# Kernel tuning notes

Hardware: AMD Instinct MI355X
Metric: run time of the kernel (lower is better)

## Reference

```python
import jax, jax.numpy as jnp
import numpy as np
import math

B, T, C, H = 2, 2048, 1024, 16
HD = C // H

def setup_inputs() -> dict:
    key = jax.random.key(0)
    ks = jax.random.split(key, 5)
    s_in = 1.0 / math.sqrt(C)
    x = jax.random.normal(ks[0], (B, T, C), dtype=jnp.float32)
    W_attn = jax.random.normal(ks[1], (C, 3 * C), dtype=jnp.float32) * s_in
    b_attn = jnp.zeros((3 * C,), dtype=jnp.float32)
    W_proj = jax.random.normal(ks[2], (C, C), dtype=jnp.float32) * s_in
    b_proj = jnp.zeros((C,), dtype=jnp.float32)
    return {"x": x, "W_attn": W_attn, "b_attn": b_attn, "W_proj": W_proj, "b_proj": b_proj}

def reference(x, W_attn, b_attn, W_proj, b_proj):
    Bx, Tx, Cx = x.shape
    c = x @ W_attn + b_attn  # [B,T,3C]
    q, k, v = jnp.split(c, 3, axis=2)
    # [B,T,H,hd] -> [B,H,T,hd]
    q = q.reshape(Bx, Tx, H, HD).transpose(0, 2, 1, 3)
    k = k.reshape(Bx, Tx, H, HD).transpose(0, 2, 1, 3)
    v = v.reshape(Bx, Tx, H, HD).transpose(0, 2, 1, 3)
    # NOTE: module scales by 1/sqrt(C), not 1/sqrt(head_dim)
    attn = jnp.einsum('bhqd,bhkd->bhqk', q, k) * (1.0 / math.sqrt(Cx))
    causal = jnp.tril(jnp.ones((Tx, Tx), dtype=bool))
    attn = jnp.where(causal[None, None], attn, -jnp.inf)
    attn = jax.nn.softmax(attn, axis=-1)
    y = jnp.einsum('bhqk,bhkd->bhqd', attn, v)
    y = y.transpose(0, 2, 1, 3).reshape(Bx, Tx, Cx)
    return y @ W_proj + b_proj
```

## Files before the change

### kernel.cpp

```cpp
#include <hip/hip_runtime.h>
#include <math.h>

#define Bv 2
#define Tv 2048
#define Cv 1024
#define Hv 16
#define HDv 64
#define Mv (Bv * Tv)
#define SZv (Bv * Hv * Tv * HDv)

typedef short bf16x8 __attribute__((ext_vector_type(8)));
typedef float f32x4 __attribute__((ext_vector_type(4)));

static __device__ __forceinline__ unsigned short f2bf(float f) {
    unsigned u = __float_as_uint(f);
    u += 0x7fffu + ((u >> 16) & 1u);
    return (unsigned short)(u >> 16);
}

static __device__ __forceinline__ unsigned f2bf2(float a, float b) {
    unsigned r;
    asm("v_cvt_pk_bf16_f32 %0, %1, %2" : "=v"(r) : "v"(a), "v"(b));
    return r;
}

#define AS1 __attribute__((address_space(1)))
#define AS3 __attribute__((address_space(3)))
#define GLD16(gp, lp) __builtin_amdgcn_global_load_lds( \
    (AS1 const void*)(const void*)(gp), (AS3 void*)(void*)(lp), 16, 0, 0)

#define WAITVM(n) asm volatile("s_waitcnt vmcnt(" #n ")" ::: "memory")
#define WAITLGKM0 asm volatile("s_waitcnt lgkmcnt(0)" ::: "memory")
#define BARRIER   asm volatile("s_barrier" ::: "memory")

__global__ __launch_bounds__(256) void cvt_kernel(
    const float* __restrict__ src, unsigned short* __restrict__ dst, int n4)
{
    int i = blockIdx.x * 256 + threadIdx.x;
    if (i < n4) {
        float4 f = ((const float4*)src)[i];
        ushort4 u;
        u.x = f2bf(f.x); u.y = f2bf(f.y); u.z = f2bf(f.z); u.w = f2bf(f.w);
        ((ushort4*)dst)[i] = u;
    }
}

__global__ __launch_bounds__(256) void transpose_kernel(
    const float* __restrict__ src, unsigned short* __restrict__ dst,
    int R, int Ncols)
{
    __shared__ float tile[32][33];
    const int c0 = blockIdx.x * 32, r0 = blockIdx.y * 32;
    const int tx = threadIdx.x & 31, ty = threadIdx.x >> 5;
    #pragma unroll
    for (int i = 0; i < 4; ++i)
        tile[ty + i * 8][tx] = src[(size_t)(r0 + ty + i * 8) * Ncols + c0 + tx];
    __syncthreads();
    #pragma unroll
    for (int i = 0; i < 4; ++i)
        dst[(size_t)(c0 + ty + i * 8) * R + r0 + tx] = f2bf(tile[tx][ty + i * 8]);
}

__device__ __forceinline__ void mm_mainloop_1024(
    const unsigned short* __restrict__ A, const unsigned short* __restrict__ Bt,
    unsigned short* lds, int rowBase, int colBase, f32x4 acc[4][4])
{
    const int tid  = threadIdx.x;
    const int lane = tid & 63;
    const int w    = tid >> 6;
    const int quad = lane >> 4, l15 = lane & 15;
    const int wm = (w >> 1) * 64, wn = (w & 1) * 64;
    const int K = 1024;

    const int g0 = (w * 2 + 0) * 64 + lane;
    const int g1 = (w * 2 + 1) * 64 + lane;
    const int r0 = g0 >> 2, r1 = g1 >> 2;
    const int kc0 = (g0 & 3) ^ ((r0 >> 1) & 3);
    const int kc1 = (g1 & 3) ^ ((r1 >> 1) & 3);
    const size_t offA0 = (size_t)(rowBase + r0) * K + kc0 * 8;
    const size_t offA1 = (size_t)(rowBase + r1) * K + kc1 * 8;
    const size_t offB0 = (size_t)(colBase + r0) * K + kc0 * 8;
    const size_t offB1 = (size_t)(colBase + r1) * K + kc1 * 8;
    unsigned short* ldsA0 = lds + (w * 2 + 0) * 512;
    unsigned short* ldsA1 = lds + (w * 2 + 1) * 512;
    unsigned short* ldsB0 = lds + 4096 + (w * 2 + 0) * 512;
    unsigned short* ldsB1 = lds + 4096 + (w * 2 + 1) * 512;

    const int sw = quad ^ ((l15 >> 1) & 3);
    int aoff[4], boff[4];
    #pragma unroll
    for (int i = 0; i < 4; ++i) {
        aoff[i] = ((wm + i * 16 + l15) * 4 + sw) * 8;
        boff[i] = 4096 + ((wn + i * 16 + l15) * 4 + sw) * 8;
    }

    GLD16(A + offA0, ldsA0);
    GLD16(A + offA1, ldsA1);
    GLD16(Bt + offB0, ldsB0);
    GLD16(Bt + offB1, ldsB1);

    for (int i = 0; i < 32; ++i) {
        const int cur = (i & 1) * 8192;
        const int nxt = 8192 - cur;
        if (i < 31) {
            const int k1 = (i + 1) * 32;
            GLD16(A + offA0 + k1, ldsA0 + nxt);
            GLD16(A + offA1 + k1, ldsA1 + nxt);
            GLD16(Bt + offB0 + k1, ldsB0 + nxt);
            GLD16(Bt + offB1 + k1, ldsB1 + nxt);
            WAITVM(4);
        } else {
            WAITVM(0);
        }
        BARRIER;

        bf16x8 a[4], b[4];
        #pragma unroll
        for (int j = 0; j < 4; ++j) a[j] = *(const bf16x8*)(lds + cur + aoff[j]);
        #pragma unroll
        for (int j = 0; j < 4; ++j) b[j] = *(const bf16x8*)(lds + cur + boff[j]);

        #pragma unroll
        for (int mi = 0; mi < 4; ++mi)
            #pragma unroll
            for (int ni = 0; ni < 4; ++ni)
                acc[mi][ni] = __builtin_amdgcn_mfma_f32_16x16x32_bf16(
                    a[mi], b[ni], acc[mi][ni], 0, 0, 0);

        WAITLGKM0;
        BARRIER;
    }
}

__global__ __launch_bounds__(256) void qkv_mm_kernel(
    const unsigned short* __restrict__ xB, const unsigned short* __restrict__ WaT,
    const float* __restrict__ bias,
    unsigned short* __restrict__ qB, unsigned short* __restrict__ kB,
    unsigned short* __restrict__ vT)
{
    __shared__ __align__(16) unsigned short lds[128 * 136];
    const int rowBase = blockIdx.y * 128;
    const int colBase = blockIdx.x * 128;

    f32x4 acc[4][4];
    #pragma unroll
    for (int i = 0; i < 4; ++i)
        #pragma unroll
        for (int j = 0; j < 4; ++j) acc[i][j] = (f32x4){0.f, 0.f, 0.f, 0.f};

    mm_mainloop_1024(xB, WaT, lds, rowBase, colBase, acc);
    __syncthreads();

    const int tid = threadIdx.x, lane = tid & 63, w = tid >> 6;
    const int quad = lane >> 4, l15 = lane & 15;
    const int wm = (w >> 1) * 64, wn = (w & 1) * 64;
    const int s = colBase / Cv;
    const int tloc = rowBase & (Tv - 1);
    const int bh0 = (rowBase / Tv) * Hv + (colBase % Cv) / HDv;

    if (s < 2) {
        const float qs = (s == 0) ? 0.04508422f : 1.0f;
        #pragma unroll
        for (int mi = 0; mi < 4; ++mi)
            #pragma unroll
            for (int ni = 0; ni < 4; ++ni) {
                float bv = bias[colBase + wn + ni * 16 + l15];
                #pragma unroll
                for (int r = 0; r < 4; ++r) {
                    int m = wm + mi * 16 + quad * 4 + r;
                    int n = wn + ni * 16 + l15;
                    lds[m * 136 + n] = f2bf((acc[mi][ni][r] + bv) * qs);
                }
            }
        __syncthreads();
        unsigned short* dst = (s == 0) ? qB : kB;
        #pragma unroll
        for (int it = 0; it < 8; ++it) {
            int cc = tid + it * 256;
            int m = cc >> 4, j = cc & 15;
            uint4 v = *(const uint4*)(lds + m * 136 + j * 8);
            int hh = j >> 3, d0 = (j & 7) * 8;
            *(uint4*)(dst + ((size_t)(bh0 + hh) * Tv + tloc + m) * HDv + d0) = v;
        }
    } else {
        #pragma unroll
        for (int mi = 0; mi < 4; ++mi)
            #pragma unroll
            for (int ni = 0; ni < 4; ++ni) {
                float bv = bias[colBase + wn + ni * 16 + l15];
                #pragma unroll
                for (int r = 0; r < 4; ++r) {
                    int m = wm + mi * 16 + quad * 4 + r;
                    int n = wn + ni * 16 + l15;
                    lds[n * 136 + m] = f2bf(acc[mi][ni][r] + bv);
                }
            }
        __syncthreads();
        #pragma unroll
        for (int it = 0; it < 8; ++it) {
            int cc = tid + it * 256;
            int n = cc >> 4, j = cc & 15;
            uint4 v = *(const uint4*)(lds + n * 136 + j * 8);
            int hh = n >> 6, d = n & 63;
            *(uint4*)(vT + ((size_t)(bh0 + hh) * HDv + d) * Tv + tloc + j * 8) = v;
        }
    }
}

__global__ __launch_bounds__(256) void proj_mm_kernel(
    const unsigned short* __restrict__ y0B, const unsigned short* __restrict__ WpT,
    const float* __restrict__ bias, float* __restrict__ out)
{
    __shared__ __align__(16) unsigned short lds[16384];
    const int rowBase = blockIdx.y * 128;
    const int colBase = blockIdx.x * 128;

    f32x4 acc[4][4];
    #pragma unroll
    for (int i = 0; i < 4; ++i)
        #pragma unroll
        for (int j = 0; j < 4; ++j) acc[i][j] = (f32x4){0.f, 0.f, 0.f, 0.f};

    mm_mainloop_1024(y0B, WpT, lds, rowBase, colBase, acc);

    const int tid = threadIdx.x, lane = tid & 63, w = tid >> 6;
    const int quad = lane >> 4, l15 = lane & 15;
    const int wm = (w >> 1) * 64, wn = (w & 1) * 64;

    #pragma unroll
    for (int mi = 0; mi < 4; ++mi)
        #pragma unroll
        for (int ni = 0; ni < 4; ++ni) {
            int n = colBase + wn + ni * 16 + l15;
            float bv = bias[n];
            #pragma unroll
            for (int r = 0; r < 4; ++r) {
                int m = rowBase + wm + mi * 16 + quad * 4 + r;
                out[(size_t)m * Cv + n] = acc[mi][ni][r] + bv;
            }
        }
}

__global__ __launch_bounds__(256) void attn_kernel(
    const unsigned short* __restrict__ qB, const unsigned short* __restrict__ kB,
    const unsigned short* __restrict__ vT, unsigned short* __restrict__ y0B)
{
    __shared__ __align__(16) unsigned short kv[2 * 8192];
    __shared__ __align__(16) unsigned short Pb[4][16 * 72];

    const int tid  = threadIdx.x;
    const int lane = tid & 63;
    const int w    = tid >> 6;
    const int quad = lane >> 4;
    const int l15  = lane & 15;

    const int qt = 31 - (blockIdx.x >> 5);
    const int bh = blockIdx.x & 31;
    const int qwbase = qt * 64 + w * 16;

    const unsigned short* qrow = qB + ((size_t)bh * Tv + qwbase + l15) * HDv;
    const bf16x8 Qa0 = *(const bf16x8*)(qrow + quad * 8);
    const bf16x8 Qa1 = *(const bf16x8*)(qrow + 32 + quad * 8);
    WAITVM(0);

    f32x4 O[4];
    float l[4] = {0.f, 0.f, 0.f, 0.f};
    #pragma unroll
    for (int n = 0; n < 4; ++n) O[n] = (f32x4){0.f, 0.f, 0.f, 0.f};

    const unsigned short* Kbase = kB + (size_t)bh * Tv * HDv;
    const unsigned short* Vbase = vT + (size_t)bh * HDv * Tv;
    unsigned short* Pw = &Pb[w][0];

    const unsigned short* gK[2]; unsigned short* dK[2];
    const unsigned short* gV[2]; unsigned short* dV[2];
    #pragma unroll
    for (int i = 0; i < 2; ++i) {
        int slot = tid + i * 256;
        int row = slot >> 3;
        int gk = (slot & 7) ^ ((row >> 2) & 7);
        gK[i] = Kbase + row * HDv + gk * 8;
        dK[i] = kv + (size_t)(i * 256 + w * 64) * 8;
        int d = slot >> 3;
        int gv = (slot & 7) ^ (d & 7);
        gV[i] = Vbase + (size_t)d * Tv + gv * 8;
        dV[i] = kv + 4096 + (size_t)(i * 256 + w * 64) * 8;
    }

    int koff[4][2], voff[4][2];
    #pragma unroll
    for (int ct = 0; ct < 4; ++ct) {
        int row = ct + 4 * l15;
        #pragma unroll
        for (int j = 0; j < 2; ++j)
            koff[ct][j] = (row * 8 + ((quad + 4 * j) ^ (l15 & 7))) * 8;
    }
    #pragma unroll
    for (int nt = 0; nt < 4; ++nt) {
        int d = nt * 16 + l15;
        #pragma unroll
        for (int j = 0; j < 2; ++j)
            voff[nt][j] = 4096 + (d * 8 + ((quad + 4 * j) ^ (l15 & 7))) * 8;
    }

    GLD16(gK[0], dK[0]);
    GLD16(gK[1], dK[1]);
    GLD16(gV[0], dV[0]);
    GLD16(gV[1], dV[1]);

    for (int kt = 0; kt <= qt; ++kt) {
        const int cur = (kt & 1) * 8192;
        const int nxt = 8192 - cur;
        if (kt < qt) {
            const int kb1 = (kt + 1) * 64;
            GLD16(gK[0] + (size_t)kb1 * HDv, dK[0] + nxt);
            GLD16(gK[1] + (size_t)kb1 * HDv, dK[1] + nxt);
            GLD16(gV[0] + kb1, dV[0] + nxt);
            GLD16(gV[1] + kb1, dV[1] + nxt);
            WAITVM(4);
        } else {
            WAITVM(0);
        }
        BARRIER;

        bf16x8 Kb[4][2], Vb[4][2];
        #pragma unroll
        for (int ct = 0; ct < 4; ++ct) {
            Kb[ct][0] = *(const bf16x8*)(kv + cur + koff[ct][0]);
            Kb[ct][1] = *(const bf16x8*)(kv + cur + koff[ct][1]);
        }
        #pragma unroll
        for (int nt = 0; nt < 4; ++nt) {
            Vb[nt][0] = *(const bf16x8*)(kv + cur + voff[nt][0]);
            Vb[nt][1] = *(const bf16x8*)(kv + cur + voff[nt][1]);
        }

        f32x4 S[4];
        #pragma unroll
        for (int ct = 0; ct < 4; ++ct) {
            S[ct] = (f32x4){0.f, 0.f, 0.f, 0.f};
            S[ct] = __builtin_amdgcn_mfma_f32_16x16x32_bf16(Qa0, Kb[ct][0], S[ct], 0, 0, 0);
            S[ct] = __builtin_amdgcn_mfma_f32_16x16x32_bf16(Qa1, Kb[ct][1], S[ct], 0, 0, 0);
        }

        if (kt == qt) {
            #pragma unroll
            for (int ct = 0; ct < 4; ++ct)
                #pragma unroll
                for (int r = 0; r < 4; ++r)
                    if (ct + 4 * l15 > w * 16 + quad * 4 + r) S[ct][r] = -1e30f;
        }

        float p[4][4];
        #pragma unroll
        for (int ct = 0; ct < 4; ++ct)
            #pragma unroll
            for (int r = 0; r < 4; ++r)
                p[ct][r] = __builtin_amdgcn_exp2f(S[ct][r]);
        #pragma unroll
        for (int r = 0; r < 4; ++r)
            l[r] += (p[0][r] + p[1][r]) + (p[2][r] + p[3][r]);

        #pragma unroll
        for (int r = 0; r < 4; ++r) {
            uint2 u = make_uint2(f2bf2(p[0][r], p[1][r]), f2bf2(p[2][r], p[3][r]));
            *(uint2*)(Pw + (quad * 4 + r) * 72 + l15 * 4) = u;
        }
        WAITLGKM0;
        const bf16x8 Pa0 = *(const bf16x8*)(Pw + l15 * 72 + quad * 8);
        const bf16x8 Pa1 = *(const bf16x8*)(Pw + l15 * 72 + 32 + quad * 8);

        #pragma unroll
        for (int nt = 0; nt < 4; ++nt) {
            O[nt] = __builtin_amdgcn_mfma_f32_16x16x32_bf16(Pa0, Vb[nt][0], O[nt], 0, 0, 0);
            O[nt] = __builtin_amdgcn_mfma_f32_16x16x32_bf16(Pa1, Vb[nt][1], O[nt], 0, 0, 0);
        }

        WAITLGKM0;
        BARRIER;
    }

    #pragma unroll
    for (int r = 0; r < 4; ++r) {
        l[r] += __shfl_xor(l[r], 1);
        l[r] += __shfl_xor(l[r], 2);
        l[r] += __shfl_xor(l[r], 4);
        l[r] += __shfl_xor(l[r], 8);
    }

    const int b = bh >> 4, h = bh & 15;
    #pragma unroll
    for (int r = 0; r < 4; ++r) {
        float inv = 1.f / l[r];
        int q = qwbase + quad * 4 + r;
        unsigned short* dst = y0B + ((size_t)(b * Tv + q)) * Cv + h * HDv + l15;
        #pragma unroll
        for (int n = 0; n < 4; ++n) dst[n * 16] = f2bf(O[n][r] * inv);
    }
}

extern "C" void kernel_launch(void* const* d_in, const int* in_sizes, int n_in,
                              void* d_out, int out_size, void* d_ws, size_t ws_size,
                              hipStream_t stream) {
    const float* x      = (const float*)d_in[0];
    const float* W_attn = (const float*)d_in[1];
    const float* b_attn = (const float*)d_in[2];
    const float* W_proj = (const float*)d_in[3];
    const float* b_proj = (const float*)d_in[4];
    float* out = (float*)d_out;

    unsigned short* xB  = (unsigned short*)d_ws;
    unsigned short* WaT = xB  + (size_t)Mv * Cv;
    unsigned short* WpT = WaT + (size_t)3 * Cv * Cv;
    unsigned short* qB  = WpT + (size_t)Cv * Cv;
    unsigned short* kB  = qB + (size_t)SZv;
    unsigned short* vT  = kB + (size_t)SZv;
    unsigned short* y0B = vT + (size_t)SZv;

    dim3 blk(256);
    cvt_kernel<<<dim3((Mv * Cv / 4) / 256), blk, 0, stream>>>(x, xB, Mv * Cv / 4);
    transpose_kernel<<<dim3(3 * Cv / 32, Cv / 32), blk, 0, stream>>>(W_attn, WaT, Cv, 3 * Cv);
    transpose_kernel<<<dim3(Cv / 32, Cv / 32), blk, 0, stream>>>(W_proj, WpT, Cv, Cv);
    qkv_mm_kernel<<<dim3(3 * Cv / 128, Mv / 128), blk, 0, stream>>>(xB, WaT, b_attn, qB, kB, vT);
    attn_kernel<<<dim3(Bv * Hv * (Tv / 64)), blk, 0, stream>>>(qB, kB, vT, y0B);
    proj_mm_kernel<<<dim3(Cv / 128, Mv / 128), blk, 0, stream>>>(y0B, WpT, b_proj, out);
}
```

Before: 181.8 us.

## Triple-buffer GEMM LDS pipeline, single-barrier attention loop, merge prep kernels

```diff
diff --git a/kernel.cpp b/kernel.cpp
--- a/kernel.cpp
+++ b/kernel.cpp
@@ -33,32 +33,37 @@
 #define WAITLGKM0 asm volatile("s_waitcnt lgkmcnt(0)" ::: "memory")
 #define BARRIER   asm volatile("s_barrier" ::: "memory")
 
-__global__ __launch_bounds__(256) void cvt_kernel(
-    const float* __restrict__ src, unsigned short* __restrict__ dst, int n4)
+__global__ __launch_bounds__(256) void prep_kernel(
+    const float* __restrict__ x, const float* __restrict__ Wa,
+    const float* __restrict__ Wp,
+    unsigned short* __restrict__ xB, unsigned short* __restrict__ WaT,
+    unsigned short* __restrict__ WpT)
 {
-    int i = blockIdx.x * 256 + threadIdx.x;
-    if (i < n4) {
-        float4 f = ((const float4*)src)[i];
+    __shared__ float tile[32][33];
+    const int bid = blockIdx.x;
+    const int tid = threadIdx.x;
+
+    if (bid < 4096) {
+        int i = bid * 256 + tid;
+        float4 f = ((const float4*)x)[i];
         ushort4 u;
         u.x = f2bf(f.x); u.y = f2bf(f.y); u.z = f2bf(f.z); u.w = f2bf(f.w);
-        ((ushort4*)dst)[i] = u;
-    }
-}
-
-__global__ __launch_bounds__(256) void transpose_kernel(
-    const float* __restrict__ src, unsigned short* __restrict__ dst,
-    int R, int Ncols)
-{
-    __shared__ float tile[32][33];
-    const int c0 = blockIdx.x * 32, r0 = blockIdx.y * 32;
-    const int tx = threadIdx.x & 31, ty = threadIdx.x >> 5;
+        ((ushort4*)xB)[i] = u;
+        return;
+    }
+    const float* src; unsigned short* dst; int Ncols, bi;
+    if (bid < 7168) { bi = bid - 4096; Ncols = 3072; src = Wa; dst = WaT; }
+    else            { bi = bid - 7168; Ncols = 1024; src = Wp; dst = WpT; }
+    const int nct = Ncols / 32;
+    const int c0 = (bi % nct) * 32, r0 = (bi / nct) * 32;
+    const int tx = tid & 31, ty = tid >> 5;
     #pragma unroll
     for (int i = 0; i < 4; ++i)
         tile[ty + i * 8][tx] = src[(size_t)(r0 + ty + i * 8) * Ncols + c0 + tx];
     __syncthreads();
     #pragma unroll
     for (int i = 0; i < 4; ++i)
-        dst[(size_t)(c0 + ty + i * 8) * R + r0 + tx] = f2bf(tile[tx][ty + i * 8]);
+        dst[(size_t)(c0 + ty + i * 8) * Cv + r0 + tx] = f2bf(tile[tx][ty + i * 8]);
 }
 
 __device__ __forceinline__ void mm_mainloop_1024(
@@ -98,21 +103,23 @@
     GLD16(A + offA1, ldsA1);
     GLD16(Bt + offB0, ldsB0);
     GLD16(Bt + offB1, ldsB1);
-
+    GLD16(A + offA0 + 32, ldsA0 + 8192);
+    GLD16(A + offA1 + 32, ldsA1 + 8192);
+    GLD16(Bt + offB0 + 32, ldsB0 + 8192);
+    GLD16(Bt + offB1 + 32, ldsB1 + 8192);
+
+    int cur = 0;
     for (int i = 0; i < 32; ++i) {
-        const int cur = (i & 1) * 8192;
-        const int nxt = 8192 - cur;
-        if (i < 31) {
-            const int k1 = (i + 1) * 32;
-            GLD16(A + offA0 + k1, ldsA0 + nxt);
-            GLD16(A + offA1 + k1, ldsA1 + nxt);
-            GLD16(Bt + offB0 + k1, ldsB0 + nxt);
-            GLD16(Bt + offB1 + k1, ldsB1 + nxt);
-            WAITVM(4);
-        } else {
-            WAITVM(0);
-        }
+        if (i < 31) { WAITVM(4); } else { WAITVM(0); }
         BARRIER;
+        if (i < 30) {
+            int nb = cur + 16384; if (nb >= 24576) nb -= 24576;
+            const int k2 = (i + 2) * 32;
+            GLD16(A + offA0 + k2, ldsA0 + nb);
+            GLD16(A + offA1 + k2, ldsA1 + nb);
+            GLD16(Bt + offB0 + k2, ldsB0 + nb);
+            GLD16(Bt + offB1 + k2, ldsB1 + nb);
+        }
 
         bf16x8 a[4], b[4];
         #pragma unroll
@@ -127,8 +134,7 @@
                 acc[mi][ni] = __builtin_amdgcn_mfma_f32_16x16x32_bf16(
                     a[mi], b[ni], acc[mi][ni], 0, 0, 0);
 
-        WAITLGKM0;
-        BARRIER;
+        cur += 8192; if (cur == 24576) cur = 0;
     }
 }
 
@@ -138,7 +144,7 @@
     unsigned short* __restrict__ qB, unsigned short* __restrict__ kB,
     unsigned short* __restrict__ vT)
 {
-    __shared__ __align__(16) unsigned short lds[128 * 136];
+    __shared__ __align__(16) unsigned short lds[24576];
     const int rowBase = blockIdx.y * 128;
     const int colBase = blockIdx.x * 128;
 
@@ -211,7 +217,7 @@
     const unsigned short* __restrict__ y0B, const unsigned short* __restrict__ WpT,
     const float* __restrict__ bias, float* __restrict__ out)
 {
-    __shared__ __align__(16) unsigned short lds[16384];
+    __shared__ __align__(16) unsigned short lds[24576];
     const int rowBase = blockIdx.y * 128;
     const int colBase = blockIdx.x * 128;
 
@@ -308,20 +314,18 @@
     GLD16(gV[0], dV[0]);
     GLD16(gV[1], dV[1]);
 
+    int cur = 0;
     for (int kt = 0; kt <= qt; ++kt) {
-        const int cur = (kt & 1) * 8192;
-        const int nxt = 8192 - cur;
+        WAITVM(0);
+        BARRIER;
         if (kt < qt) {
             const int kb1 = (kt + 1) * 64;
+            const int nxt = 8192 - cur;
             GLD16(gK[0] + (size_t)kb1 * HDv, dK[0] + nxt);
             GLD16(gK[1] + (size_t)kb1 * HDv, dK[1] + nxt);
             GLD16(gV[0] + kb1, dV[0] + nxt);
             GLD16(gV[1] + kb1, dV[1] + nxt);
-            WAITVM(4);
-        } else {
-            WAITVM(0);
-        }
-        BARRIER;
+        }
 
         bf16x8 Kb[4][2], Vb[4][2];
         #pragma unroll
@@ -376,8 +380,7 @@
             O[nt] = __builtin_amdgcn_mfma_f32_16x16x32_bf16(Pa1, Vb[nt][1], O[nt], 0, 0, 0);
         }
 
-        WAITLGKM0;
-        BARRIER;
+        cur = 8192 - cur;
     }
 
     #pragma unroll
@@ -418,9 +421,7 @@
     unsigned short* y0B = vT + (size_t)SZv;
 
     dim3 blk(256);
-    cvt_kernel<<<dim3((Mv * Cv / 4) / 256), blk, 0, stream>>>(x, xB, Mv * Cv / 4);
-    transpose_kernel<<<dim3(3 * Cv / 32, Cv / 32), blk, 0, stream>>>(W_attn, WaT, Cv, 3 * Cv);
-    transpose_kernel<<<dim3(Cv / 32, Cv / 32), blk, 0, stream>>>(W_proj, WpT, Cv, Cv);
+    prep_kernel<<<dim3(8192), blk, 0, stream>>>(x, W_attn, W_proj, xB, WaT, WpT);
     qkv_mm_kernel<<<dim3(3 * Cv / 128, Mv / 128), blk, 0, stream>>>(xB, WaT, b_attn, qB, kB, vT);
     attn_kernel<<<dim3(Bv * Hv * (Tv / 64)), blk, 0, stream>>>(qB, kB, vT, y0B);
     proj_mm_kernel<<<dim3(Cv / 128, Mv / 128), blk, 0, stream>>>(y0B, WpT, b_proj, out);
```

Measured after the change: 169.2 us. 1.07x faster.
